# Kernel tuning notes

Measured on AMD Instinct MI355X. Metric: run time of the kernel, lower is better.

## Reference

```python
import jax, jax.numpy as jnp
import numpy as np

CAPACITY_FACTOR = 1.0  # fairseq Top1Gate default


def setup_inputs() -> dict:
    key = jax.random.key(0)
    ks = jax.random.split(key, 5)
    B, T, M, H, O, E = 8, 1024, 1024, 4096, 1024, 4
    return {
        "hidden_states": jax.random.normal(ks[0], (B, T, M), jnp.float32),
        "gate_w": jax.random.normal(ks[1], (M, E), jnp.float32) * 0.02,
        "fc1_w": jax.random.normal(ks[2], (E, M, H), jnp.float32) * 0.02,
        "fc1_b": jnp.zeros((E, H), jnp.float32),
        "fc2_w": jax.random.normal(ks[3], (E, H, O), jnp.float32) * 0.02,
        "fc2_b": jnp.zeros((E, O), jnp.float32),
    }


def reference(hidden_states, gate_w, fc1_w, fc1_b, fc2_w, fc2_b):
    B, T, M = hidden_states.shape
    E = gate_w.shape[1]
    S = B * T
    C = int(CAPACITY_FACTOR * -(-S // E))  # ceil(S/E)

    features = hidden_states.reshape(S, M)  # [S, M]

    # ---- Top1 gate (fairseq top1gating, eval path: no shuffle/noise) ----
    logits = features @ gate_w                      # [S, E]
    gates = jax.nn.softmax(logits, axis=1)          # [S, E]
    idx = jnp.argmax(gates, axis=1)                 # [S]
    mask1 = jax.nn.one_hot(idx, E, dtype=gates.dtype)  # [S, E]

    # load-balancing aux loss (computed before capacity dropping)
    me = jnp.mean(gates, axis=0)
    ce = jnp.mean(mask1, axis=0)
    l_aux = jnp.sum(me * ce) * E

    # capacity: position within each expert's queue; drop overflow tokens
    locations = jnp.cumsum(mask1, axis=0) - 1.0     # [S, E]
    mask1 = mask1 * (locations < C)
    loc_s = jnp.sum(locations * mask1, axis=1).astype(jnp.int32)  # [S]
    gates1_s = jnp.sum(gates * mask1, axis=1)       # [S] gate value (0 if dropped)

    # combine_weights [S, E, C] and boolean dispatch mask (as float for mm)
    combine = (gates1_s[:, None, None] * mask1[:, :, None]
               * jax.nn.one_hot(loc_s, C, dtype=gates.dtype)[:, None, :])
    dispatch = (combine > 0).astype(features.dtype)  # [S, E, C]

    # ---- dispatch via dense one-hot matmul: [E*C, S] @ [S, M] ----
    dispatch_ecs = jnp.transpose(dispatch, (1, 2, 0)).reshape(E * C, S)
    dispatched = (dispatch_ecs @ features).reshape(E, C, M)

    # ---- per-expert MLP (grouped GEMM) ----
    h = jax.nn.gelu(jnp.einsum('ecm,emh->ech', dispatched, fc1_w) + fc1_b[:, None, :])
    expert_out = jnp.einsum('ech,eho->eco', h, fc2_w) + fc2_b[:, None, :]  # [E, C, O]

    # ---- combine via dense matmul: [S, E*C] @ [E*C, O] ----
    O = expert_out.shape[-1]
    combined = combine.reshape(S, E * C) @ expert_out.reshape(E * C, O)

    return combined.reshape(B, T, O), l_aux
```

## Files before the change

### kernel.cpp

```cpp
#include <hip/hip_runtime.h>
#include <stdint.h>

#define S_TOK 8192
#define MDIM  1024
#define HDIM  4096
#define ODIM  1024
#define NEXP  4
#define CAP   2048

typedef __attribute__((ext_vector_type(8))) short short8;
typedef __attribute__((ext_vector_type(4))) float floatx4;

__device__ __forceinline__ unsigned short f2bf(float x) {
  union { float f; unsigned u; } v; v.f = x;
  unsigned r = v.u + 0x7FFFu + ((v.u >> 16) & 1u);
  return (unsigned short)(r >> 16);
}

__device__ __forceinline__ void gl_lds16(const void* g, void* l) {
  __builtin_amdgcn_global_load_lds(
      (const __attribute__((address_space(1))) void*)g,
      (__attribute__((address_space(3))) void*)l, 16, 0, 0);
}

__device__ __forceinline__ float gelu_tanh(float x) {
  float z = 0.7978845608028654f * (x + 0.044715f * x * x * x);
  float t = 1.0f - 2.0f / (__expf(2.0f * z) + 1.0f);
  return 0.5f * x * (1.0f + t);
}

__device__ __forceinline__ const char* stage_src(const char* base, int linoff,
                                                 int rowstride) {
  int row  = linoff >> 6;
  int slot = (linoff >> 4) & 3;
  int c16  = slot ^ ((row >> 1) & 3);
  return base + (size_t)row * rowstride + (c16 << 4);
}

__global__ __launch_bounds__(256) void gate_kernel(
    const float* __restrict__ feat, const float* __restrict__ gw,
    int* __restrict__ idx, float* __restrict__ gval, float* __restrict__ gsum)
{
  int wave = threadIdx.x >> 6, lane = threadIdx.x & 63;
  int s = blockIdx.x * 4 + wave;
  const float* f = feat + (size_t)s * MDIM;
  double a0 = 0, a1 = 0, a2 = 0, a3 = 0;
  #pragma unroll
  for (int j = 0; j < 16; ++j) {
    int m = lane + j * 64;
    float x = f[m];
    float4 w = ((const float4*)gw)[m];
    a0 += (double)x * w.x; a1 += (double)x * w.y;
    a2 += (double)x * w.z; a3 += (double)x * w.w;
  }
  #pragma unroll
  for (int off = 32; off; off >>= 1) {
    a0 += __shfl_down(a0, off); a1 += __shfl_down(a1, off);
    a2 += __shfl_down(a2, off); a3 += __shfl_down(a3, off);
  }
  __shared__ float bs[4];
  if (threadIdx.x < 4) bs[threadIdx.x] = 0.f;
  __syncthreads();
  if (lane == 0) {
    double lg[4] = {a0, a1, a2, a3};
    double mx = lg[0]; int bi = 0;
    #pragma unroll
    for (int e = 1; e < 4; ++e) if (lg[e] > mx) { mx = lg[e]; bi = e; }
    float ex[4]; float den = 0.f;
    #pragma unroll
    for (int e = 0; e < 4; ++e) { ex[e] = __expf((float)(lg[e] - mx)); den += ex[e]; }
    float inv = 1.f / den;
    idx[s]  = bi;
    gval[s] = ex[bi] * inv;
    #pragma unroll
    for (int e = 0; e < 4; ++e) atomicAdd(&bs[e], ex[e] * inv);
  }
  __syncthreads();
  if (threadIdx.x < 4) atomicAdd(&gsum[threadIdx.x], bs[threadIdx.x]);
}

__global__ __launch_bounds__(1024) void scan_kernel(
    const int* __restrict__ idx, int* __restrict__ perm,
    int* __restrict__ ne, const float* __restrict__ gsum,
    float* __restrict__ laux)
{
  const int tid = threadIdx.x, wave = tid >> 6, lane = tid & 63;
  __shared__ int cnt[16][4];
  __shared__ int off[16][4];
  __shared__ int tot[4];
  unsigned long long below = (lane == 0) ? 0ull : ((~0ull) >> (64 - lane));

  int myE[8], loc[8];
  int c[4] = {0, 0, 0, 0};
  #pragma unroll
  for (int j = 0; j < 8; ++j) {
    int s = wave * 512 + j * 64 + lane;
    int ev = idx[s];
    myE[j] = ev;
    #pragma unroll
    for (int e = 0; e < 4; ++e) {
      unsigned long long mb = __ballot(ev == e);
      if (ev == e) loc[j] = c[e] + __popcll(mb & below);
      c[e] += __popcll(mb);
    }
  }
  if (lane == 0) {
    #pragma unroll
    for (int e = 0; e < 4; ++e) cnt[wave][e] = c[e];
  }
  __syncthreads();
  if (tid < 64) {
    int w = tid >> 2, e = tid & 3;
    int o = 0;
    for (int w2 = 0; w2 < 16; ++w2) if (w2 < w) o += cnt[w2][e];
    off[w][e] = o;
    if (w == 15) tot[e] = o + cnt[15][e];
  }
  __syncthreads();
  #pragma unroll
  for (int j = 0; j < 8; ++j) {
    int s = wave * 512 + j * 64 + lane;
    int e = myE[j];
    int rank = off[wave][e] + loc[j];
    if (rank < CAP) perm[e * CAP + rank] = s;
  }
  if (tid < 4) ne[tid] = tot[tid] < CAP ? tot[tid] : CAP;
  if (tid == 0) {
    float l = 0.f;
    #pragma unroll
    for (int e = 0; e < 4; ++e)
      l += (gsum[e] * (1.0f / S_TOK)) * ((float)tot[e] * (1.0f / S_TOK));
    *laux = l * (float)NEXP;
  }
}

__global__ __launch_bounds__(256) void transpose_cast(
    const float* __restrict__ in, unsigned short* __restrict__ out, int R, int Cc)
{
  __shared__ unsigned short tile[64][66];
  in  += (size_t)blockIdx.z * R * Cc;
  out += (size_t)blockIdx.z * R * Cc;
  int c0 = blockIdx.x * 64, r0 = blockIdx.y * 64;
  int tx = threadIdx.x & 15;
  int ty = threadIdx.x >> 4;
  #pragma unroll
  for (int p = 0; p < 4; ++p) {
    int r = ty + p * 16;
    float4 v = *(const float4*)(in + (size_t)(r0 + r) * Cc + c0 + tx * 4);
    tile[r][tx * 4 + 0] = f2bf(v.x);
    tile[r][tx * 4 + 1] = f2bf(v.y);
    tile[r][tx * 4 + 2] = f2bf(v.z);
    tile[r][tx * 4 + 3] = f2bf(v.w);
  }
  __syncthreads();
  #pragma unroll
  for (int p = 0; p < 4; ++p) {
    int c = ty + p * 16;
    ushort4 o;
    o.x = tile[tx * 4 + 0][c];
    o.y = tile[tx * 4 + 1][c];
    o.z = tile[tx * 4 + 2][c];
    o.w = tile[tx * 4 + 3][c];
    *(ushort4*)(out + (size_t)(c0 + c) * R + r0 + tx * 4) = o;
  }
}

__global__ __launch_bounds__(256) void gather_kernel(
    const float* __restrict__ feat, const int* __restrict__ perm,
    const int* __restrict__ ne, unsigned short* __restrict__ disp)
{
  int b = blockIdx.x;
  int e = b >> 11, c = b & (CAP - 1);
  int m = threadIdx.x * 4;
  ushort4 o;
  if (c < ne[e]) {
    int s = perm[b];
    float4 v = *(const float4*)(feat + (size_t)s * MDIM + m);
    o.x = f2bf(v.x); o.y = f2bf(v.y); o.z = f2bf(v.z); o.w = f2bf(v.w);
  } else {
    o.x = o.y = o.z = o.w = 0;
  }
  *(ushort4*)(disp + (size_t)b * MDIM + m) = o;
}

__global__ __launch_bounds__(256) void fc1_kernel(
    const unsigned short* __restrict__ A, const unsigned short* __restrict__ Bt,
    const float* __restrict__ b1, unsigned short* __restrict__ Hb)
{
  const int b = blockIdx.x;
  const int wg = (b & 7) * 256 + (b >> 3);
  const int nb = wg & 31, mb = (wg >> 5) & 15, e = wg >> 9;
  const int tid = threadIdx.x, wave = tid >> 6, lane = tid & 63;

  __shared__ __align__(16) unsigned short smA[3 * 128 * 32];
  __shared__ __align__(16) unsigned short smB[3 * 128 * 32];

  const char* Ag = (const char*)(A + ((size_t)e * CAP + (size_t)mb * 128) * MDIM);
  const char* Bg = (const char*)(Bt + ((size_t)e * HDIM + (size_t)nb * 128) * MDIM);

  const int boff0 = (wave * 2 + 0) * 1024 + lane * 16;
  const int boff1 = (wave * 2 + 1) * 1024 + lane * 16;
  const char* agp0 = stage_src(Ag, boff0, 2048);
  const char* agp1 = stage_src(Ag, boff1, 2048);
  const char* bgp0 = stage_src(Bg, boff0, 2048);
  const char* bgp1 = stage_src(Bg, boff1, 2048);
  const int ldsw0 = (wave * 2 + 0) * 512;
  const int ldsw1 = (wave * 2 + 1) * 512;

  const int wm = (wave & 1) * 64, wn = (wave >> 1) * 64;
  const int fr = lane & 15, fq = lane >> 4;
  const int sqA = ((fq ^ ((wm + fr) >> 1)) & 3) * 8;
  const int sqB = ((fq ^ ((wn + fr) >> 1)) & 3) * 8;

  floatx4 acc[4][4] = {};

  const int NT = MDIM / 32;
  int c0 = 0, c1 = 1, c2 = 2;

  gl_lds16(agp0 + 0,  smA + 0 * 4096 + ldsw0);
  gl_lds16(agp1 + 0,  smA + 0 * 4096 + ldsw1);
  gl_lds16(bgp0 + 0,  smB + 0 * 4096 + ldsw0);
  gl_lds16(bgp1 + 0,  smB + 0 * 4096 + ldsw1);
  gl_lds16(agp0 + 64, smA + 1 * 4096 + ldsw0);
  gl_lds16(agp1 + 64, smA + 1 * 4096 + ldsw1);
  gl_lds16(bgp0 + 64, smB + 1 * 4096 + ldsw0);
  gl_lds16(bgp1 + 64, smB + 1 * 4096 + ldsw1);
  asm volatile("s_waitcnt vmcnt(4)" ::: "memory");
  __builtin_amdgcn_s_barrier();

  for (int kt = 0; kt < NT; ++kt) {
    if (kt + 2 < NT) {
      int kb = (kt + 2) * 64;
      gl_lds16(agp0 + kb, smA + c2 * 4096 + ldsw0);
      gl_lds16(agp1 + kb, smA + c2 * 4096 + ldsw1);
      gl_lds16(bgp0 + kb, smB + c2 * 4096 + ldsw0);
      gl_lds16(bgp1 + kb, smB + c2 * 4096 + ldsw1);
    }
    const unsigned short* sA = smA + c0 * 4096;
    const unsigned short* sB = smB + c0 * 4096;
    short8 af[4], bfr[4];
    #pragma unroll
    for (int i = 0; i < 4; ++i)
      af[i] = *(const short8*)&sA[(wm + i * 16 + fr) * 32 + sqA];
    #pragma unroll
    for (int j = 0; j < 4; ++j)
      bfr[j] = *(const short8*)&sB[(wn + j * 16 + fr) * 32 + sqB];
    #pragma unroll
    for (int i = 0; i < 4; ++i)
      #pragma unroll
      for (int j = 0; j < 4; ++j)
        acc[i][j] = __builtin_amdgcn_mfma_f32_16x16x32_bf16(af[i], bfr[j], acc[i][j], 0, 0, 0);
    if (kt + 1 < NT) {
      if (kt + 2 < NT) asm volatile("s_waitcnt vmcnt(4)" ::: "memory");
      else             asm volatile("s_waitcnt vmcnt(0)" ::: "memory");
      __builtin_amdgcn_s_barrier();
    }
    int t = c0; c0 = c1; c1 = c2; c2 = t;
  }

  unsigned short* Hrow = Hb + (size_t)e * CAP * HDIM;
  #pragma unroll
  for (int j = 0; j < 4; ++j) {
    int gn = nb * 128 + wn + j * 16 + fr;
    float bv = b1[e * HDIM + gn];
    #pragma unroll
    for (int i = 0; i < 4; ++i) {
      int m0 = mb * 128 + wm + i * 16 + fq * 4;
      #pragma unroll
      for (int r = 0; r < 4; ++r)
        Hrow[(size_t)(m0 + r) * HDIM + gn] = f2bf(gelu_tanh(acc[i][j][r] + bv));
    }
  }
}

__global__ __launch_bounds__(256) void fc2_kernel(
    const unsigned short* __restrict__ A, const unsigned short* __restrict__ Bt,
    const float* __restrict__ b2, const int* __restrict__ perm,
    const int* __restrict__ ne, const float* __restrict__ gval,
    float* __restrict__ out)
{
  const int b = blockIdx.x;
  const int wg = (b & 7) * 128 + (b >> 3);
  const int nb = wg & 7, mb = (wg >> 3) & 31, e = wg >> 8;
  const int tid = threadIdx.x, wave = tid >> 6, lane = tid & 63;

  __shared__ __align__(16) unsigned short smA[3 * 64 * 32];
  __shared__ __align__(16) unsigned short smB[3 * 128 * 32];

  const char* Ag = (const char*)(A + ((size_t)e * CAP + (size_t)mb * 64) * HDIM);
  const char* Bg = (const char*)(Bt + ((size_t)e * ODIM + (size_t)nb * 128) * HDIM);

  const char* agp = stage_src(Ag, tid * 16, 8192);
  const int boff0 = (wave * 2 + 0) * 1024 + lane * 16;
  const int boff1 = (wave * 2 + 1) * 1024 + lane * 16;
  const char* bgp0 = stage_src(Bg, boff0, 8192);
  const char* bgp1 = stage_src(Bg, boff1, 8192);

  const int ldsA_w = wave * 512;
  const int ldsB_w0 = (wave * 2 + 0) * 512;
  const int ldsB_w1 = (wave * 2 + 1) * 512;

  const int wm = (wave & 1) * 32, wn = (wave >> 1) * 64;
  const int fr = lane & 15, fq = lane >> 4;
  const int sqA = ((fq ^ ((wm + fr) >> 1)) & 3) * 8;
  const int sqB = ((fq ^ ((wn + fr) >> 1)) & 3) * 8;

  floatx4 acc[2][4] = {};

  const int NT = HDIM / 32;
  int c0 = 0, c1 = 1, c2 = 2;

  gl_lds16(agp + 0 * 64,  smA + 0 * 2048 + ldsA_w);
  gl_lds16(bgp0 + 0 * 64, smB + 0 * 4096 + ldsB_w0);
  gl_lds16(bgp1 + 0 * 64, smB + 0 * 4096 + ldsB_w1);
  gl_lds16(agp + 1 * 64,  smA + 1 * 2048 + ldsA_w);
  gl_lds16(bgp0 + 1 * 64, smB + 1 * 4096 + ldsB_w0);
  gl_lds16(bgp1 + 1 * 64, smB + 1 * 4096 + ldsB_w1);
  asm volatile("s_waitcnt vmcnt(3)" ::: "memory");
  __builtin_amdgcn_s_barrier();

  for (int kt = 0; kt < NT; ++kt) {
    if (kt + 2 < NT) {
      int kb = (kt + 2) * 64;
      gl_lds16(agp + kb,  smA + c2 * 2048 + ldsA_w);
      gl_lds16(bgp0 + kb, smB + c2 * 4096 + ldsB_w0);
      gl_lds16(bgp1 + kb, smB + c2 * 4096 + ldsB_w1);
    }
    const unsigned short* sA = smA + c0 * 2048;
    const unsigned short* sB = smB + c0 * 4096;
    short8 af[2], bfr[4];
    #pragma unroll
    for (int i = 0; i < 2; ++i)
      af[i] = *(const short8*)&sA[(wm + i * 16 + fr) * 32 + sqA];
    #pragma unroll
    for (int j = 0; j < 4; ++j)
      bfr[j] = *(const short8*)&sB[(wn + j * 16 + fr) * 32 + sqB];
    #pragma unroll
    for (int i = 0; i < 2; ++i)
      #pragma unroll
      for (int j = 0; j < 4; ++j)
        acc[i][j] = __builtin_amdgcn_mfma_f32_16x16x32_bf16(af[i], bfr[j], acc[i][j], 0, 0, 0);
    if (kt + 1 < NT) {
      if (kt + 2 < NT) asm volatile("s_waitcnt vmcnt(3)" ::: "memory");
      else             asm volatile("s_waitcnt vmcnt(0)" ::: "memory");
      __builtin_amdgcn_s_barrier();
    }
    int t = c0; c0 = c1; c1 = c2; c2 = t;
  }

  const int nE = ne[e];
  float b2v[4];
  #pragma unroll
  for (int j = 0; j < 4; ++j)
    b2v[j] = b2[e * ODIM + nb * 128 + wn + j * 16 + fr];
  #pragma unroll
  for (int i = 0; i < 2; ++i) {
    #pragma unroll
    for (int r = 0; r < 4; ++r) {
      int c = mb * 64 + wm + i * 16 + fq * 4 + r;
      if (c < nE) {
        int s = perm[e * CAP + c];
        float g = gval[s];
        float* orow = out + (size_t)s * ODIM + nb * 128 + wn;
        #pragma unroll
        for (int j = 0; j < 4; ++j)
          orow[j * 16 + fr] = (acc[i][j][r] + b2v[j]) * g;
      }
    }
  }
}

extern "C" void kernel_launch(void* const* d_in, const int* in_sizes, int n_in,
                              void* d_out, int out_size, void* d_ws, size_t ws_size,
                              hipStream_t stream) {
  const float* feat = (const float*)d_in[0];
  const float* gw   = (const float*)d_in[1];
  const float* w1   = (const float*)d_in[2];
  const float* b1   = (const float*)d_in[3];
  const float* w2   = (const float*)d_in[4];
  const float* b2   = (const float*)d_in[5];
  float* out = (float*)d_out;

  char* ws = (char*)d_ws;
  unsigned short* wt   = (unsigned short*)(ws);
  unsigned short* hbuf = (unsigned short*)(ws + 33554432);
  unsigned short* disp = (unsigned short*)(ws + 100663296);
  int*   idx  = (int*)  (ws + 117440512);
  float* gval = (float*)(ws + 117473280);
  int*   perm = (int*)  (ws + 117506048);
  float* gsum = (float*)(ws + 117538816);
  int*   ne   = (int*)  (ws + 117538832);

  hipMemsetAsync(d_out, 0, (size_t)S_TOK * ODIM * sizeof(float), stream);
  hipMemsetAsync(ws + 117538816, 0, 32, stream);

  gate_kernel<<<S_TOK / 4, 256, 0, stream>>>(feat, gw, idx, gval, gsum);
  scan_kernel<<<1, 1024, 0, stream>>>(idx, perm, ne, gsum, out + (size_t)S_TOK * ODIM);
  transpose_cast<<<dim3(HDIM / 64, MDIM / 64, NEXP), 256, 0, stream>>>(w1, wt, MDIM, HDIM);
  gather_kernel<<<NEXP * CAP, 256, 0, stream>>>(feat, perm, ne, disp);
  fc1_kernel<<<2048, 256, 0, stream>>>(disp, wt, b1, hbuf);
  transpose_cast<<<dim3(ODIM / 64, HDIM / 64, NEXP), 256, 0, stream>>>(w2, wt, HDIM, ODIM);
  fc2_kernel<<<1024, 256, 0, stream>>>(hbuf, wt, b2, perm, ne, gval, out);
}
```

Baseline: 442.4 us.

## Swap MFMA operands for vectorized row-contiguous epilogue stores and simplify GELU

Result: no change. 435.2 us (-1.6%).

```diff
diff --git a/kernel.cpp b/kernel.cpp
--- a/kernel.cpp
+++ b/kernel.cpp
@@ -24,9 +24,10 @@
 }
 
 __device__ __forceinline__ float gelu_tanh(float x) {
-  float z = 0.7978845608028654f * (x + 0.044715f * x * x * x);
-  float t = 1.0f - 2.0f / (__expf(2.0f * z) + 1.0f);
-  return 0.5f * x * (1.0f + t);
+  float p = x * x;
+  float t = x * (1.5957691216f + 0.0713548353f * p);
+  float E = __expf(-t);
+  return __fdividef(x, 1.0f + E);
 }
 
 __device__ __forceinline__ const char* stage_src(const char* base, int linoff,
@@ -187,9 +188,7 @@
     const unsigned short* __restrict__ A, const unsigned short* __restrict__ Bt,
     const float* __restrict__ b1, unsigned short* __restrict__ Hb)
 {
-  const int b = blockIdx.x;
-  const int wg = (b & 7) * 256 + (b >> 3);
-  const int nb = wg & 31, mb = (wg >> 5) & 15, e = wg >> 9;
+  const int nb = blockIdx.x, mb = blockIdx.y, e = blockIdx.z;
   const int tid = threadIdx.x, wave = tid >> 6, lane = tid & 63;
 
   __shared__ __align__(16) unsigned short smA[3 * 128 * 32];
@@ -249,7 +248,7 @@
     for (int i = 0; i < 4; ++i)
       #pragma unroll
       for (int j = 0; j < 4; ++j)
-        acc[i][j] = __builtin_amdgcn_mfma_f32_16x16x32_bf16(af[i], bfr[j], acc[i][j], 0, 0, 0);
+        acc[i][j] = __builtin_amdgcn_mfma_f32_16x16x32_bf16(bfr[j], af[i], acc[i][j], 0, 0, 0);
     if (kt + 1 < NT) {
       if (kt + 2 < NT) asm volatile("s_waitcnt vmcnt(4)" ::: "memory");
       else             asm volatile("s_waitcnt vmcnt(0)" ::: "memory");
@@ -261,14 +260,17 @@
   unsigned short* Hrow = Hb + (size_t)e * CAP * HDIM;
   #pragma unroll
   for (int j = 0; j < 4; ++j) {
-    int gn = nb * 128 + wn + j * 16 + fr;
-    float bv = b1[e * HDIM + gn];
+    int gn0 = nb * 128 + wn + j * 16 + fq * 4;
+    float4 bv = *(const float4*)&b1[e * HDIM + gn0];
     #pragma unroll
     for (int i = 0; i < 4; ++i) {
-      int m0 = mb * 128 + wm + i * 16 + fq * 4;
-      #pragma unroll
-      for (int r = 0; r < 4; ++r)
-        Hrow[(size_t)(m0 + r) * HDIM + gn] = f2bf(gelu_tanh(acc[i][j][r] + bv));
+      int m = mb * 128 + wm + i * 16 + fr;
+      ushort4 o;
+      o.x = f2bf(gelu_tanh(acc[i][j][0] + bv.x));
+      o.y = f2bf(gelu_tanh(acc[i][j][1] + bv.y));
+      o.z = f2bf(gelu_tanh(acc[i][j][2] + bv.z));
+      o.w = f2bf(gelu_tanh(acc[i][j][3] + bv.w));
+      *(ushort4*)&Hrow[(size_t)m * HDIM + gn0] = o;
     }
   }
 }
@@ -339,7 +341,7 @@
     for (int i = 0; i < 2; ++i)
       #pragma unroll
       for (int j = 0; j < 4; ++j)
-        acc[i][j] = __builtin_amdgcn_mfma_f32_16x16x32_bf16(af[i], bfr[j], acc[i][j], 0, 0, 0);
+        acc[i][j] = __builtin_amdgcn_mfma_f32_16x16x32_bf16(bfr[j], af[i], acc[i][j], 0, 0, 0);
     if (kt + 1 < NT) {
       if (kt + 2 < NT) asm volatile("s_waitcnt vmcnt(3)" ::: "memory");
       else             asm volatile("s_waitcnt vmcnt(0)" ::: "memory");
@@ -349,22 +351,25 @@
   }
 
   const int nE = ne[e];
-  float b2v[4];
+  float4 b2v[4];
   #pragma unroll
   for (int j = 0; j < 4; ++j)
-    b2v[j] = b2[e * ODIM + nb * 128 + wn + j * 16 + fr];
+    b2v[j] = *(const float4*)&b2[e * ODIM + nb * 128 + wn + j * 16 + fq * 4];
   #pragma unroll
   for (int i = 0; i < 2; ++i) {
-    #pragma unroll
-    for (int r = 0; r < 4; ++r) {
-      int c = mb * 64 + wm + i * 16 + fq * 4 + r;
-      if (c < nE) {
-        int s = perm[e * CAP + c];
-        float g = gval[s];
-        float* orow = out + (size_t)s * ODIM + nb * 128 + wn;
-        #pragma unroll
-        for (int j = 0; j < 4; ++j)
-          orow[j * 16 + fr] = (acc[i][j][r] + b2v[j]) * g;
+    int c = mb * 64 + wm + i * 16 + fr;
+    if (c < nE) {
+      int s = perm[e * CAP + c];
+      float g = gval[s];
+      float* orow = out + (size_t)s * ODIM + nb * 128 + wn + fq * 4;
+      #pragma unroll
+      for (int j = 0; j < 4; ++j) {
+        float4 o;
+        o.x = (acc[i][j][0] + b2v[j].x) * g;
+        o.y = (acc[i][j][1] + b2v[j].y) * g;
+        o.z = (acc[i][j][2] + b2v[j].z) * g;
+        o.w = (acc[i][j][3] + b2v[j].w) * g;
+        *(float4*)&orow[j * 16] = o;
       }
     }
   }
@@ -398,7 +403,7 @@
   scan_kernel<<<1, 1024, 0, stream>>>(idx, perm, ne, gsum, out + (size_t)S_TOK * ODIM);
   transpose_cast<<<dim3(HDIM / 64, MDIM / 64, NEXP), 256, 0, stream>>>(w1, wt, MDIM, HDIM);
   gather_kernel<<<NEXP * CAP, 256, 0, stream>>>(feat, perm, ne, disp);
-  fc1_kernel<<<2048, 256, 0, stream>>>(disp, wt, b1, hbuf);
+  fc1_kernel<<<dim3(HDIM / 128, CAP / 128, NEXP), 256, 0, stream>>>(disp, wt, b1, hbuf);
   transpose_cast<<<dim3(ODIM / 64, HDIM / 64, NEXP), 256, 0, stream>>>(w2, wt, HDIM, ODIM);
   fc2_kernel<<<1024, 256, 0, stream>>>(hbuf, wt, b2, perm, ne, gval, out);
 }
```
